# Kernel optimization log

Measured on AMD Instinct MI355X. Metric: run time of the kernel, lower is better.

The kernel has to match this reference:

```python
import jax, jax.numpy as jnp
import numpy as np

DIM = 4096

def _fwht_unnormalized(y):
    # y: (T, d), iterative radix-2 butterfly, unnormalized Sylvester WHT
    d = y.shape[-1]
    h = 1
    while h < d:
        y = y.reshape(-1, d // (2 * h), 2, h)
        a = y[..., 0, :]
        b = y[..., 1, :]
        y = jnp.stack([a + b, a - b], axis=-2).reshape(-1, d)
        h *= 2
    return y

def setup_inputs() -> dict:
    key = jax.random.key(0)
    x = jax.random.normal(key, (4, 2048, DIM), dtype=jnp.float32)
    return {"x": x}

def reference(x):
    # Original: x_flat @ H.T where H is built recursively with a 1/sqrt(n)
    # division at EVERY recursion level. H is symmetric, and equals the
    # unnormalized Sylvester Hadamard times 2^{-L(L+1)/4}, L = log2(d).
    shape = x.shape
    d = shape[-1]
    L = int(round(np.log2(d)))
    scale = np.float32(2.0 ** (-(L * (L + 1)) / 4.0))
    y = _fwht_unnormalized(x.reshape(-1, d))
    return (y * scale).reshape(shape)
```

## Files before the change

### kernel.cpp

```cpp
#include <hip/hip_runtime.h>


constexpr int DIM = 4096;

__device__ __forceinline__ void fwht16(float v[16]) {
#pragma unroll
    for (int h = 1; h < 16; h <<= 1) {
#pragma unroll
        for (int i = 0; i < 16; i += 2 * h) {
#pragma unroll
            for (int k = 0; k < h; ++k) {
                float a = v[i + k];
                float b = v[i + k + h];
                v[i + k]     = a + b;
                v[i + k + h] = a - b;
            }
        }
    }
}

__global__ __launch_bounds__(256, 8) void fwht4096_kernel(const float* __restrict__ x,
                                                          float* __restrict__ y) {
    __shared__ float buf[17 * 256];
    const int t = threadIdx.x;
    const long long row = blockIdx.x;
    const int t_hi = t >> 4;
    const int t_lo = t & 15;

    float v[16];

    {
        const float4* src = reinterpret_cast<const float4*>(x + row * DIM + t * 16);
#pragma unroll
        for (int q = 0; q < 4; ++q) {
            float4 f = src[q];
            v[4 * q + 0] = f.x;
            v[4 * q + 1] = f.y;
            v[4 * q + 2] = f.z;
            v[4 * q + 3] = f.w;
        }
    }

    fwht16(v);

    {
        float* wp = buf + 17 * t;
#pragma unroll
        for (int j = 0; j < 16; ++j) wp[j] = v[j];
    }
    __syncthreads();
    {
        const float* rp = buf + 272 * t_hi + t_lo;
#pragma unroll
        for (int j = 0; j < 16; ++j) v[j] = rp[17 * j];
    }

    fwht16(v);

    __syncthreads();

    {
        float* wp = buf + 17 * t_lo + t_hi;
#pragma unroll
        for (int j = 0; j < 16; ++j) wp[272 * j] = v[j];
    }
    __syncthreads();
    {
        const float* rp = buf + 17 * t;
#pragma unroll
        for (int j = 0; j < 16; ++j) v[j] = rp[j];
    }

    fwht16(v);

    const float scale = 0x1p-39f;
    float* dst = y + row * DIM + t;
#pragma unroll
    for (int j = 0; j < 16; ++j) {
        dst[j * 256] = v[j] * scale;
    }
}

extern "C" void kernel_launch(void* const* d_in, const int* in_sizes, int n_in,
                              void* d_out, int out_size, void* d_ws, size_t ws_size,
                              hipStream_t stream) {
    const float* x = (const float*)d_in[0];
    float* y = (float*)d_out;
    const int nrows = in_sizes[0] / DIM;
    fwht4096_kernel<<<nrows, 256, 0, stream>>>(x, y);
}
```

Baseline: 226.6 us.

## Use persistent grid-stride blocks with register prefetch of next row and nontemporal stores

The launch now uses at most 2048 blocks, and each block loops over rows with a grid stride. While processing the current row, each block loads the next row into registers so the global-memory latency overlaps with the shared-memory transposes and butterflies. Output stores become nontemporal to reduce cache pollution. This adds register pressure from the prefetch buffer and an extra barrier per iteration, and with 8192 rows each block handles only four rows.

```diff
diff --git a/kernel.cpp b/kernel.cpp
--- a/kernel.cpp
+++ b/kernel.cpp
@@ -2,6 +2,8 @@
 
 
 constexpr int DIM = 4096;
+constexpr int PITCH = 17;
+constexpr int NBLOCKS = 2048;
 
 __device__ __forceinline__ void fwht16(float v[16]) {
 #pragma unroll
@@ -20,64 +22,81 @@
 }
 
 __global__ __launch_bounds__(256, 8) void fwht4096_kernel(const float* __restrict__ x,
-                                                          float* __restrict__ y) {
-    __shared__ float buf[17 * 256];
+                                                          float* __restrict__ y,
+                                                          int nrows) {
+    __shared__ float buf[PITCH * 256];
     const int t = threadIdx.x;
-    const long long row = blockIdx.x;
     const int t_hi = t >> 4;
     const int t_lo = t & 15;
 
-    float v[16];
-
-    {
+    float4 nxt[4];
+    long long row = blockIdx.x;
+    if (row < nrows) {
         const float4* src = reinterpret_cast<const float4*>(x + row * DIM + t * 16);
 #pragma unroll
-        for (int q = 0; q < 4; ++q) {
-            float4 f = src[q];
-            v[4 * q + 0] = f.x;
-            v[4 * q + 1] = f.y;
-            v[4 * q + 2] = f.z;
-            v[4 * q + 3] = f.w;
-        }
+        for (int q = 0; q < 4; ++q) nxt[q] = src[q];
     }
 
-    fwht16(v);
+    for (; row < nrows; row += NBLOCKS) {
+        float v[16];
+#pragma unroll
+        for (int q = 0; q < 4; ++q) {
+            v[4 * q + 0] = nxt[q].x;
+            v[4 * q + 1] = nxt[q].y;
+            v[4 * q + 2] = nxt[q].z;
+            v[4 * q + 3] = nxt[q].w;
+        }
 
-    {
-        float* wp = buf + 17 * t;
+        fwht16(v);
+
+        __syncthreads();
+
+        {
+            float* wp = buf + PITCH * t;
 #pragma unroll
-        for (int j = 0; j < 16; ++j) wp[j] = v[j];
-    }
-    __syncthreads();
-    {
-        const float* rp = buf + 272 * t_hi + t_lo;
+            for (int j = 0; j < 16; ++j) wp[j] = v[j];
+        }
+        __syncthreads();
+        {
+            const float* rp = buf + (PITCH * 16) * t_hi + t_lo;
 #pragma unroll
-        for (int j = 0; j < 16; ++j) v[j] = rp[17 * j];
-    }
+            for (int j = 0; j < 16; ++j) v[j] = rp[PITCH * j];
+        }
 
-    fwht16(v);
+        fwht16(v);
 
-    __syncthreads();
+        {
+            const long long nrow = row + NBLOCKS;
+            if (nrow < nrows) {
+                const float4* src =
+                    reinterpret_cast<const float4*>(x + nrow * DIM + t * 16);
+#pragma unroll
+                for (int q = 0; q < 4; ++q) nxt[q] = src[q];
+            }
+        }
 
-    {
-        float* wp = buf + 17 * t_lo + t_hi;
+        __syncthreads();
+
+        {
+            float* wp = buf + PITCH * t_lo + t_hi;
 #pragma unroll
-        for (int j = 0; j < 16; ++j) wp[272 * j] = v[j];
-    }
-    __syncthreads();
-    {
-        const float* rp = buf + 17 * t;
+            for (int j = 0; j < 16; ++j) wp[(PITCH * 16) * j] = v[j];
+        }
+        __syncthreads();
+        {
+            const float* rp = buf + PITCH * t;
 #pragma unroll
-        for (int j = 0; j < 16; ++j) v[j] = rp[j];
-    }
+            for (int j = 0; j < 16; ++j) v[j] = rp[j];
+        }
 
-    fwht16(v);
+        fwht16(v);
 
-    const float scale = 0x1p-39f;
-    float* dst = y + row * DIM + t;
+        const float scale = 0x1p-39f;
+        float* dst = y + row * DIM + t;
 #pragma unroll
-    for (int j = 0; j < 16; ++j) {
-        dst[j * 256] = v[j] * scale;
+        for (int j = 0; j < 16; ++j) {
+            __builtin_nontemporal_store(v[j] * scale, dst + j * 256);
+        }
     }
 }
 
@@ -87,5 +106,6 @@
     const float* x = (const float*)d_in[0];
     float* y = (float*)d_out;
     const int nrows = in_sizes[0] / DIM;
-    fwht4096_kernel<<<nrows, 256, 0, stream>>>(x, y);
+    const int grid = nrows < NBLOCKS ? nrows : NBLOCKS;
+    fwht4096_kernel<<<grid, 256, 0, stream>>>(x, y, nrows);
 }
```

After: 231.1 us. Within noise of the previous version (+2.0%).

## Process two rows per block with interleaved transforms and nontemporal stores

Applied to the files above, without the earlier changes.

Each block now handles two rows, each with its own shared-memory buffer. Both rows' loads are issued up front, and the FWHT stages and LDS transposes of the two rows are interleaved so one row's arithmetic can overlap the other's LDS traffic. The first transpose drops its barrier, because every value read there was written by a thread in the same 64-lane wavefront. Output stores become nontemporal and the launch-bounds occupancy hint drops from 8 to 4, in exchange for more registers and LDS per block and half as many blocks.

```diff
diff --git a/kernel.cpp b/kernel.cpp
--- a/kernel.cpp
+++ b/kernel.cpp
@@ -2,6 +2,7 @@
 
 
 constexpr int DIM = 4096;
+constexpr int P1 = 17;
 
 __device__ __forceinline__ void fwht16(float v[16]) {
 #pragma unroll
@@ -19,65 +20,109 @@
     }
 }
 
-__global__ __launch_bounds__(256, 8) void fwht4096_kernel(const float* __restrict__ x,
+__global__ __launch_bounds__(256, 4) void fwht4096_kernel(const float* __restrict__ x,
                                                           float* __restrict__ y) {
-    __shared__ float buf[17 * 256];
+    __shared__ float P[P1 * 256];
+    __shared__ float Q[P1 * 256];
     const int t = threadIdx.x;
-    const long long row = blockIdx.x;
     const int t_hi = t >> 4;
     const int t_lo = t & 15;
+    const long long r0 = 2LL * blockIdx.x;
 
-    float v[16];
+    float u[16], w[16];
+
+    float4 La[4], Lb[4];
+    {
+        const float4* s0 = reinterpret_cast<const float4*>(x + r0 * DIM + t * 16);
+        const float4* s1 = reinterpret_cast<const float4*>(x + (r0 + 1) * DIM + t * 16);
+#pragma unroll
+        for (int q = 0; q < 4; ++q) La[q] = s0[q];
+#pragma unroll
+        for (int q = 0; q < 4; ++q) Lb[q] = s1[q];
+    }
+
+#pragma unroll
+    for (int q = 0; q < 4; ++q) {
+        u[4 * q + 0] = La[q].x; u[4 * q + 1] = La[q].y;
+        u[4 * q + 2] = La[q].z; u[4 * q + 3] = La[q].w;
+    }
+    fwht16(u);
 
     {
-        const float4* src = reinterpret_cast<const float4*>(x + row * DIM + t * 16);
+        float* wp = P + P1 * t;
 #pragma unroll
-        for (int q = 0; q < 4; ++q) {
-            float4 f = src[q];
-            v[4 * q + 0] = f.x;
-            v[4 * q + 1] = f.y;
-            v[4 * q + 2] = f.z;
-            v[4 * q + 3] = f.w;
-        }
+        for (int j = 0; j < 16; ++j) wp[j] = u[j];
+        const float* rp = P + (P1 * 16) * t_hi + t_lo;
+#pragma unroll
+        for (int j = 0; j < 16; ++j) u[j] = rp[P1 * j];
     }
 
-    fwht16(v);
+#pragma unroll
+    for (int q = 0; q < 4; ++q) {
+        w[4 * q + 0] = Lb[q].x; w[4 * q + 1] = Lb[q].y;
+        w[4 * q + 2] = Lb[q].z; w[4 * q + 3] = Lb[q].w;
+    }
+    fwht16(w);
+
+    fwht16(u);
 
     {
-        float* wp = buf + 17 * t;
+        float* wp = Q + P1 * t;
 #pragma unroll
-        for (int j = 0; j < 16; ++j) wp[j] = v[j];
+        for (int j = 0; j < 16; ++j) wp[j] = w[j];
+        const float* rp = Q + (P1 * 16) * t_hi + t_lo;
+#pragma unroll
+        for (int j = 0; j < 16; ++j) w[j] = rp[P1 * j];
     }
-    __syncthreads();
-    {
-        const float* rp = buf + 272 * t_hi + t_lo;
-#pragma unroll
-        for (int j = 0; j < 16; ++j) v[j] = rp[17 * j];
-    }
-
-    fwht16(v);
 
     __syncthreads();
 
     {
-        float* wp = buf + 17 * t_lo + t_hi;
+        float* wp = P + P1 * t_lo + t_hi;
 #pragma unroll
-        for (int j = 0; j < 16; ++j) wp[272 * j] = v[j];
-    }
-    __syncthreads();
-    {
-        const float* rp = buf + 17 * t;
-#pragma unroll
-        for (int j = 0; j < 16; ++j) v[j] = rp[j];
+        for (int j = 0; j < 16; ++j) wp[(P1 * 16) * j] = u[j];
     }
 
-    fwht16(v);
+    fwht16(w);
+
+    __syncthreads();
+
+    {
+        const float* rp = P + P1 * t;
+#pragma unroll
+        for (int j = 0; j < 16; ++j) u[j] = rp[j];
+    }
+    {
+        float* wp = Q + P1 * t_lo + t_hi;
+#pragma unroll
+        for (int j = 0; j < 16; ++j) wp[(P1 * 16) * j] = w[j];
+    }
+
+    fwht16(u);
+
+    __syncthreads();
+
+    {
+        const float* rp = Q + P1 * t;
+#pragma unroll
+        for (int j = 0; j < 16; ++j) w[j] = rp[j];
+    }
 
     const float scale = 0x1p-39f;
-    float* dst = y + row * DIM + t;
+    {
+        float* dst = y + r0 * DIM + t;
 #pragma unroll
-    for (int j = 0; j < 16; ++j) {
-        dst[j * 256] = v[j] * scale;
+        for (int j = 0; j < 16; ++j)
+            __builtin_nontemporal_store(u[j] * scale, dst + j * 256);
+    }
+
+    fwht16(w);
+
+    {
+        float* dst = y + (r0 + 1) * DIM + t;
+#pragma unroll
+        for (int j = 0; j < 16; ++j)
+            __builtin_nontemporal_store(w[j] * scale, dst + j * 256);
     }
 }
 
@@ -87,5 +132,5 @@
     const float* x = (const float*)d_in[0];
     float* y = (float*)d_out;
     const int nrows = in_sizes[0] / DIM;
-    fwht4096_kernel<<<nrows, 256, 0, stream>>>(x, y);
+    fwht4096_kernel<<<nrows / 2, 256, 0, stream>>>(x, y);
 }
```

New measurement: 228.6 us. No clear change (+0.9%).
